# Optimization experiments

Measured on AMD Instinct MI355X. Metric: run time of the kernel, lower is better.

Reference implementation:

```python
import jax, jax.numpy as jnp
import numpy as np

BINS = 1024
DIM = 128
B, T = 8, 32768


def setup_inputs() -> dict:
    key = jax.random.key(0)
    k1, k2 = jax.random.split(key)
    hidden_states = jax.random.normal(k1, (B, T, DIM), dtype=jnp.float32)
    embed = jax.random.normal(k2, (BINS, DIM), dtype=jnp.float32)
    return {"hidden_states": hidden_states, "embed": embed}


def reference(hidden_states, embed):
    # encode: flatten to [N, dim], nearest codebook entry by Euclidean distance
    shape = hidden_states.shape
    x = hidden_states.reshape(-1, shape[-1])                    # [N, dim]
    x_sq = jnp.sum(x * x, axis=1, keepdims=True)                # [N, 1]
    e_sq = jnp.sum(embed * embed, axis=1)[None, :]              # [1, bins]
    dist = -(x_sq - 2.0 * (x @ embed.T) + e_sq)                 # [N, bins]
    embed_ind = jnp.argmax(dist, axis=-1)                       # [N]
    embed_ind = embed_ind.reshape(shape[:-1])                   # [B, T]
    # decode: embedding gather
    quantize = embed[embed_ind]                                 # [B, T, dim]
    return quantize, embed_ind
```

## Files before the change

kernel.cpp:

```cpp
#include <hip/hip_runtime.h>

#define DIM  128
#define BINS 1024

typedef __attribute__((ext_vector_type(8))) _Float16 f16x8;
typedef __attribute__((ext_vector_type(4))) float f32x4;

#define MFMA16(a, b, c) __builtin_amdgcn_mfma_f32_16x16x32_f16(a, b, c, 0, 0, 0)

#define GLDS(gp, lp) __builtin_amdgcn_global_load_lds(                        \
    (const __attribute__((address_space(1))) void*)(gp),                     \
    (__attribute__((address_space(3))) void*)(lp), 16, 0, 0)

__device__ __forceinline__ float med3a(float a, float b, float c) {
    float r;
    asm("v_med3_f32 %0, %1, %2, %3" : "=v"(r) : "v"(a), "v"(b), "v"(c));
    return r;
}

__device__ __forceinline__ float packkey(float k, int bin) {
    float r;
    asm("v_and_or_b32 %0, %1, %2, %3"
        : "=v"(r) : "v"(k), "s"(0xFFFFFC00u), "v"(bin));
    return r;
}

#define SINS(x, S0, S1, S2, S3) do {                                          \
        float n0_ = fmaxf(S0, (x));                                           \
        float n1_ = med3a((x), S0, S1);                                       \
        float n2_ = med3a((x), S1, S2);                                       \
        float n3_ = med3a((x), S2, S3);                                       \
        S0 = n0_; S1 = n1_; S2 = n2_; S3 = n3_;                               \
    } while (0)

__global__ __launch_bounds__(256) void vq_prep(
    const float* __restrict__ embed, _Float16* __restrict__ ehs,
    float* __restrict__ esq_g, float* __restrict__ cinit_g)
{
    int b = blockIdx.x * 256 + threadIdx.x;
    const float* e = embed + (size_t)b * DIM;
    float s = 0.f;
    #pragma unroll
    for (int k = 0; k < DIM; ++k) s = fmaf(e[k], e[k], s);
    esq_g[b] = s;
    cinit_g[b] = -0.5f * s;
    #pragma unroll
    for (int c = 0; c < 16; ++c) {
        int slot = c ^ (b & 15);
        #pragma unroll
        for (int j = 0; j < 8; ++j)
            ehs[b * 128 + slot * 8 + j] = (_Float16)e[c * 8 + j];
    }
}

__global__ __launch_bounds__(256) void vq_stage_a(
    const float* __restrict__ x,
    const _Float16* __restrict__ ehs_g,
    const float* __restrict__ cinit_g,
    float* __restrict__ cand)
{
    __shared__ _Float16 ehb[2][8192];
    __shared__ float ci_lds[BINS];

    const int tid = threadIdx.x;
    const int li  = tid & 15;
    const int g   = (tid >> 4) & 3;
    const int w   = tid >> 6;

    f16x8 xh[2][4];
    const size_t rowA = (size_t)blockIdx.x * 128 + w * 32 + li;
    #pragma unroll
    for (int rs = 0; rs < 2; ++rs) {
        const float* xp = x + (rowA + rs * 16) * DIM + g * 8;
        #pragma unroll
        for (int s = 0; s < 4; ++s) {
            float4 v0 = *(const float4*)(xp + s * 32);
            float4 v1 = *(const float4*)(xp + s * 32 + 4);
            f16x8 h;
            h[0] = (_Float16)v0.x; h[1] = (_Float16)v0.y;
            h[2] = (_Float16)v0.z; h[3] = (_Float16)v0.w;
            h[4] = (_Float16)v1.x; h[5] = (_Float16)v1.y;
            h[6] = (_Float16)v1.z; h[7] = (_Float16)v1.w;
            xh[rs][s] = h;
        }
    }

#define STAGE(stp_, buf_) do {                                                \
        const char* gE_ = (const char*)ehs_g + (size_t)(stp_) * 16384;        \
        char* lE_ = (char*)&ehb[buf_][0];                                     \
        _Pragma("unroll")                                                     \
        for (int j_ = 0; j_ < 4; ++j_) {                                      \
            int o_ = tid * 16 + j_ * 4096;                                    \
            GLDS(gE_ + o_, lE_ + o_);                                         \
        }                                                                     \
    } while (0)

    GLDS((const char*)cinit_g + tid * 16, (char*)ci_lds + tid * 16);
    STAGE(0, 0);
    asm volatile("s_waitcnt vmcnt(0)" ::: "memory");
    __syncthreads();

    const float NEG = __uint_as_float(0xFF7FFC00u);
    float s0[2], s1[2], s2[2], s3[2];
    #pragma unroll
    for (int rs = 0; rs < 2; ++rs) { s0[rs] = s1[rs] = s2[rs] = s3[rs] = NEG; }

#define LDE(tl_, s_) (*(const f16x8*)((const char*)&ehb[buf][0] + (tl_) * 4096 + li * 256 + (((g + 4 * (s_)) ^ li) << 4)))

    for (int stp = 0; stp < 16; ++stp) {
        const int buf = stp & 1;
        if (stp < 15) STAGE(stp + 1, buf ^ 1);

        #pragma unroll
        for (int tl = 0; tl < 4; ++tl) {
            const int binb = stp * 64 + tl * 16 + g * 4;
            const f32x4 ci = *(const f32x4*)&ci_lds[binb];
            f16x8 eh0 = LDE(tl, 0), eh1 = LDE(tl, 1);
            f16x8 eh2 = LDE(tl, 2), eh3 = LDE(tl, 3);
            f32x4 aP0 = MFMA16(eh0, xh[0][0], ci);
            f32x4 aP1 = MFMA16(eh0, xh[1][0], ci);
            aP0 = MFMA16(eh1, xh[0][1], aP0); aP1 = MFMA16(eh1, xh[1][1], aP1);
            aP0 = MFMA16(eh2, xh[0][2], aP0); aP1 = MFMA16(eh2, xh[1][2], aP1);
            aP0 = MFMA16(eh3, xh[0][3], aP0); aP1 = MFMA16(eh3, xh[1][3], aP1);
            {
                float p0 = packkey(aP0[0], binb + 0);
                float p1 = packkey(aP0[1], binb + 1);
                float p2 = packkey(aP0[2], binb + 2);
                float p3 = packkey(aP0[3], binb + 3);
                float pm01 = fmaxf(p0, p1), pm23 = fmaxf(p2, p3);
                SINS(pm01, s0[0], s1[0], s2[0], s3[0]);
                SINS(pm23, s0[0], s1[0], s2[0], s3[0]);
            }
            {
                float p0 = packkey(aP1[0], binb + 0);
                float p1 = packkey(aP1[1], binb + 1);
                float p2 = packkey(aP1[2], binb + 2);
                float p3 = packkey(aP1[3], binb + 3);
                float pm01 = fmaxf(p0, p1), pm23 = fmaxf(p2, p3);
                SINS(pm01, s0[1], s1[1], s2[1], s3[1]);
                SINS(pm23, s0[1], s1[1], s2[1], s3[1]);
            }
        }
        asm volatile("s_waitcnt vmcnt(0)" ::: "memory");
        __syncthreads();
    }
#undef LDE
#undef STAGE

    #pragma unroll
    for (int mm = 16; mm <= 32; mm <<= 1) {
        #pragma unroll
        for (int rs = 0; rs < 2; ++rs) {
            float q0 = __shfl_xor(s0[rs], mm);
            float q1 = __shfl_xor(s1[rs], mm);
            float q2 = __shfl_xor(s2[rs], mm);
            float q3 = __shfl_xor(s3[rs], mm);
            SINS(q0, s0[rs], s1[rs], s2[rs], s3[rs]);
            SINS(q1, s0[rs], s1[rs], s2[rs], s3[rs]);
            SINS(q2, s0[rs], s1[rs], s2[rs], s3[rs]);
            SINS(q3, s0[rs], s1[rs], s2[rs], s3[rs]);
        }
    }
    if ((tid & 63) < 16) {
        #pragma unroll
        for (int rs = 0; rs < 2; ++rs) {
            const size_t r = rowA + rs * 16;
            cand[r * 4 + 0] = (float)(__float_as_uint(s0[rs]) & 1022u);
            cand[r * 4 + 1] = (float)(__float_as_uint(s1[rs]) & 1022u);
            cand[r * 4 + 2] = (float)(__float_as_uint(s2[rs]) & 1022u);
            cand[r * 4 + 3] = (float)(__float_as_uint(s3[rs]) & 1022u);
        }
    }
}

__global__ __launch_bounds__(256) void vq_rescore(
    const float* __restrict__ x, const float* __restrict__ embed,
    const float* __restrict__ esq_g, const float* __restrict__ cand,
    float* __restrict__ ind_f, float4* __restrict__ outq)
{
    const int tid = threadIdx.x;
    const int sub = tid & 3;
    const size_t row = (size_t)blockIdx.x * 64 + (tid >> 2);

    const float4* xg = (const float4*)(x + row * DIM);
    float4 xq[8];
    #pragma unroll
    for (int j = 0; j < 8; ++j) xq[j] = xg[j * 4 + sub];

    float xs = 0.f;
    #pragma unroll
    for (int j = 0; j < 8; ++j) {
        float4 v = xq[j];
        xs = fmaf(v.x, v.x, xs); xs = fmaf(v.y, v.y, xs);
        xs = fmaf(v.z, v.z, xs); xs = fmaf(v.w, v.w, xs);
    }
    xs += __shfl_xor(xs, 1);
    xs += __shfl_xor(xs, 2);

    const float4 qv = *(const float4*)&cand[row * 4];
    const int qb0 = (int)qv.x, qb1 = (int)qv.y, qb2 = (int)qv.z, qb3 = (int)qv.w;

    const float4* e4 = (const float4*)embed;
    f32x4 acc[8];
    #pragma unroll
    for (int c = 0; c < 8; ++c) acc[c] = f32x4{0.f,0.f,0.f,0.f};
    #pragma unroll
    for (int c = 0; c < 8; ++c) {
        const int bin = (c < 2 ? qb0 : c < 4 ? qb1 : c < 6 ? qb2 : qb3) + (c & 1);
        #pragma unroll
        for (int j = 0; j < 8; ++j) {
            float4 ev = e4[(size_t)bin * 32 + j * 4 + sub];
            float4 xv = xq[j];
            acc[c][0] = fmaf(xv.x, ev.x, acc[c][0]);
            acc[c][1] = fmaf(xv.y, ev.y, acc[c][1]);
            acc[c][2] = fmaf(xv.z, ev.z, acc[c][2]);
            acc[c][3] = fmaf(xv.w, ev.w, acc[c][3]);
        }
    }
    float bd = -3.402823466e38f;
    int   bb = 0x7FFFFFFF;
    #pragma unroll
    for (int c = 0; c < 8; ++c) {
        const int bin = (c < 2 ? qb0 : c < 4 ? qb1 : c < 6 ? qb2 : qb3) + (c & 1);
        float p = (acc[c][0] + acc[c][1]) + (acc[c][2] + acc[c][3]);
        p += __shfl_xor(p, 1);
        p += __shfl_xor(p, 2);
        float d = -(fmaf(-2.f, p, xs) + esq_g[bin]);
        if (d > bd || (d == bd && bin < bb)) { bd = d; bb = bin; }
    }
    if (sub == 0) ind_f[row] = (float)bb;
    if (outq) {
        #pragma unroll
        for (int j = 0; j < 8; ++j)
            outq[row * 32 + j * 4 + sub] = e4[(size_t)bb * 32 + j * 4 + sub];
    }
}

__global__ __launch_bounds__(256) void vq_gather(
    const float* __restrict__ embed,
    const float* __restrict__ ind_f,
    float4* __restrict__ out)
{
    int i   = blockIdx.x * 256 + threadIdx.x;
    int row = i >> 5;
    int k   = i & 31;
    int b   = (int)ind_f[row];
    out[i] = reinterpret_cast<const float4*>(embed)[b * (DIM / 4) + k];
}

extern "C" void kernel_launch(void* const* d_in, const int* in_sizes, int n_in,
                              void* d_out, int out_size, void* d_ws, size_t ws_size,
                              hipStream_t stream) {
    const float* x     = (const float*)d_in[0];
    const float* embed = (const float*)d_in[1];
    float* out = (float*)d_out;

    const int N = in_sizes[0] / DIM;
    float* ind_f = out + (size_t)N * DIM;

    const bool use_ws = ws_size >= ((size_t)6 << 20);
    _Float16* ehs; float* esq_g; float* cinit_g; float* cand;
    if (use_ws) {
        char* wb = (char*)d_ws;
        ehs     = (_Float16*)wb;
        esq_g   = (float*)(wb + (256u << 10));
        cinit_g = (float*)(wb + (260u << 10));
        cand    = (float*)(wb + (512u << 10));
    } else {
        char* ob = (char*)d_out;
        cand    = out;
        ehs     = (_Float16*)(ob + (32u << 20));
        esq_g   = (float*)(ob + (36u << 20));
        cinit_g = (float*)(ob + (36u << 20) + 4096);
    }

    vq_prep<<<BINS / 256, 256, 0, stream>>>(embed, ehs, esq_g, cinit_g);
    vq_stage_a<<<N / 128, 256, 0, stream>>>(x, ehs, cinit_g, cand);
    vq_rescore<<<N / 64, 256, 0, stream>>>(x, embed, esq_g, cand, ind_f,
                                           use_ws ? (float4*)out : nullptr);
    if (!use_ws)
        vq_gather<<<(N * (DIM / 4)) / 256, 256, 0, stream>>>(embed, ind_f, (float4*)out);
}
```

Measured before the change: 188.5 us.

## Use 1024-thread blocks staging half the codebook at once in stage A

Stage A now runs 1024-thread blocks covering 512 rows, and loads half the fp16 codebook (128KB) into LDS in two phases instead of double-buffering 16KB slices with a barrier per slice. This cuts the number of barriers and reuses each staged codebook tile across four times as many rows. The cinit bias is read straight from global instead of LDS. The key packing now does the max of each bin pair before packing a 9-bit pair id, which saves packkey ops. The cost is a single block per CU with no overlap between loads and compute, and the coarser key gives less mantissa precision for the candidate shortlist.

```diff
diff --git a/kernel.cpp b/kernel.cpp
--- a/kernel.cpp
+++ b/kernel.cpp
@@ -18,10 +18,10 @@
     return r;
 }
 
-__device__ __forceinline__ float packkey(float k, int bin) {
+__device__ __forceinline__ float packkey(float k, int pid) {
     float r;
     asm("v_and_or_b32 %0, %1, %2, %3"
-        : "=v"(r) : "v"(k), "s"(0xFFFFFC00u), "v"(bin));
+        : "=v"(r) : "v"(k), "s"(0xFFFFFE00u), "v"(pid));
     return r;
 }
 
@@ -53,22 +53,22 @@
     }
 }
 
-__global__ __launch_bounds__(256) void vq_stage_a(
+__global__ __launch_bounds__(1024, 1) void vq_stage_a(
     const float* __restrict__ x,
     const _Float16* __restrict__ ehs_g,
     const float* __restrict__ cinit_g,
     float* __restrict__ cand)
 {
-    __shared__ _Float16 ehb[2][8192];
-    __shared__ float ci_lds[BINS];
-
-    const int tid = threadIdx.x;
-    const int li  = tid & 15;
-    const int g   = (tid >> 4) & 3;
-    const int w   = tid >> 6;
+    __shared__ _Float16 ehb[65536];
+
+    const int tid  = threadIdx.x;
+    const int lane = tid & 63;
+    const int li   = lane & 15;
+    const int g    = lane >> 4;
+    const int w    = tid >> 6;
 
     f16x8 xh[2][4];
-    const size_t rowA = (size_t)blockIdx.x * 128 + w * 32 + li;
+    const size_t rowA = (size_t)blockIdx.x * 512 + w * 32 + li;
     #pragma unroll
     for (int rs = 0; rs < 2; ++rs) {
         const float* xp = x + (rowA + rs * 16) * DIM + g * 8;
@@ -85,67 +85,59 @@
         }
     }
 
-#define STAGE(stp_, buf_) do {                                                \
-        const char* gE_ = (const char*)ehs_g + (size_t)(stp_) * 16384;        \
-        char* lE_ = (char*)&ehb[buf_][0];                                     \
-        _Pragma("unroll")                                                     \
-        for (int j_ = 0; j_ < 4; ++j_) {                                      \
-            int o_ = tid * 16 + j_ * 4096;                                    \
-            GLDS(gE_ + o_, lE_ + o_);                                         \
-        }                                                                     \
-    } while (0)
-
-    GLDS((const char*)cinit_g + tid * 16, (char*)ci_lds + tid * 16);
-    STAGE(0, 0);
-    asm volatile("s_waitcnt vmcnt(0)" ::: "memory");
-    __syncthreads();
-
-    const float NEG = __uint_as_float(0xFF7FFC00u);
+    int off0 = li * 256 + (((g + 0)  ^ li) << 4);
+    int off1 = li * 256 + (((g + 4)  ^ li) << 4);
+    int off2 = li * 256 + (((g + 8)  ^ li) << 4);
+    int off3 = li * 256 + (((g + 12) ^ li) << 4);
+    const float* cip = cinit_g + g * 4;
+
+    const float NEG = __uint_as_float(0xFF7FFE00u);
     float s0[2], s1[2], s2[2], s3[2];
     #pragma unroll
     for (int rs = 0; rs < 2; ++rs) { s0[rs] = s1[rs] = s2[rs] = s3[rs] = NEG; }
 
-#define LDE(tl_, s_) (*(const f16x8*)((const char*)&ehb[buf][0] + (tl_) * 4096 + li * 256 + (((g + 4 * (s_)) ^ li) << 4)))
-
-    for (int stp = 0; stp < 16; ++stp) {
-        const int buf = stp & 1;
-        if (stp < 15) STAGE(stp + 1, buf ^ 1);
-
-        #pragma unroll
-        for (int tl = 0; tl < 4; ++tl) {
-            const int binb = stp * 64 + tl * 16 + g * 4;
-            const f32x4 ci = *(const f32x4*)&ci_lds[binb];
-            f16x8 eh0 = LDE(tl, 0), eh1 = LDE(tl, 1);
-            f16x8 eh2 = LDE(tl, 2), eh3 = LDE(tl, 3);
-            f32x4 aP0 = MFMA16(eh0, xh[0][0], ci);
-            f32x4 aP1 = MFMA16(eh0, xh[1][0], ci);
-            aP0 = MFMA16(eh1, xh[0][1], aP0); aP1 = MFMA16(eh1, xh[1][1], aP1);
-            aP0 = MFMA16(eh2, xh[0][2], aP0); aP1 = MFMA16(eh2, xh[1][2], aP1);
-            aP0 = MFMA16(eh3, xh[0][3], aP0); aP1 = MFMA16(eh3, xh[1][3], aP1);
+    for (int p = 0; p < 2; ++p) {
+        if (p) __syncthreads();
+        {
+            const char* gsrc = (const char*)ehs_g + (size_t)p * 131072;
+            char* ldst = (char*)&ehb[0];
+            int o = tid * 16;
+            #pragma unroll
+            for (int sl = 0; sl < 8; ++sl)
+                GLDS(gsrc + sl * 16384 + o, ldst + sl * 16384 + o);
+        }
+        asm volatile("s_waitcnt vmcnt(0)" ::: "memory");
+        __syncthreads();
+
+        #pragma unroll 4
+        for (int tt = 0; tt < 32; ++tt) {
+            const int t = p * 32 + tt;
+            const char* bE = (const char*)&ehb[0] + tt * 4096;
+            f16x8 e0 = *(const f16x8*)(bE + off0);
+            f16x8 e1 = *(const f16x8*)(bE + off1);
+            f16x8 e2 = *(const f16x8*)(bE + off2);
+            f16x8 e3 = *(const f16x8*)(bE + off3);
+            const f32x4 ci = *(const f32x4*)(cip + t * 16);
+            f32x4 aP0 = MFMA16(e0, xh[0][0], ci);
+            f32x4 aP1 = MFMA16(e0, xh[1][0], ci);
+            aP0 = MFMA16(e1, xh[0][1], aP0); aP1 = MFMA16(e1, xh[1][1], aP1);
+            aP0 = MFMA16(e2, xh[0][2], aP0); aP1 = MFMA16(e2, xh[1][2], aP1);
+            aP0 = MFMA16(e3, xh[0][3], aP0); aP1 = MFMA16(e3, xh[1][3], aP1);
+            const int pid = t * 8 + g * 2;
             {
-                float p0 = packkey(aP0[0], binb + 0);
-                float p1 = packkey(aP0[1], binb + 1);
-                float p2 = packkey(aP0[2], binb + 2);
-                float p3 = packkey(aP0[3], binb + 3);
-                float pm01 = fmaxf(p0, p1), pm23 = fmaxf(p2, p3);
-                SINS(pm01, s0[0], s1[0], s2[0], s3[0]);
-                SINS(pm23, s0[0], s1[0], s2[0], s3[0]);
+                float q01 = packkey(fmaxf(aP0[0], aP0[1]), pid);
+                float q23 = packkey(fmaxf(aP0[2], aP0[3]), pid + 1);
+                SINS(q01, s0[0], s1[0], s2[0], s3[0]);
+                SINS(q23, s0[0], s1[0], s2[0], s3[0]);
             }
             {
-                float p0 = packkey(aP1[0], binb + 0);
-                float p1 = packkey(aP1[1], binb + 1);
-                float p2 = packkey(aP1[2], binb + 2);
-                float p3 = packkey(aP1[3], binb + 3);
-                float pm01 = fmaxf(p0, p1), pm23 = fmaxf(p2, p3);
-                SINS(pm01, s0[1], s1[1], s2[1], s3[1]);
-                SINS(pm23, s0[1], s1[1], s2[1], s3[1]);
+                float q01 = packkey(fmaxf(aP1[0], aP1[1]), pid);
+                float q23 = packkey(fmaxf(aP1[2], aP1[3]), pid + 1);
+                SINS(q01, s0[1], s1[1], s2[1], s3[1]);
+                SINS(q23, s0[1], s1[1], s2[1], s3[1]);
             }
         }
-        asm volatile("s_waitcnt vmcnt(0)" ::: "memory");
-        __syncthreads();
-    }
-#undef LDE
-#undef STAGE
+    }
 
     #pragma unroll
     for (int mm = 16; mm <= 32; mm <<= 1) {
@@ -161,14 +153,14 @@
             SINS(q3, s0[rs], s1[rs], s2[rs], s3[rs]);
         }
     }
-    if ((tid & 63) < 16) {
+    if (lane < 16) {
         #pragma unroll
         for (int rs = 0; rs < 2; ++rs) {
             const size_t r = rowA + rs * 16;
-            cand[r * 4 + 0] = (float)(__float_as_uint(s0[rs]) & 1022u);
-            cand[r * 4 + 1] = (float)(__float_as_uint(s1[rs]) & 1022u);
-            cand[r * 4 + 2] = (float)(__float_as_uint(s2[rs]) & 1022u);
-            cand[r * 4 + 3] = (float)(__float_as_uint(s3[rs]) & 1022u);
+            cand[r * 4 + 0] = (float)((__float_as_uint(s0[rs]) & 0x1FFu) << 1);
+            cand[r * 4 + 1] = (float)((__float_as_uint(s1[rs]) & 0x1FFu) << 1);
+            cand[r * 4 + 2] = (float)((__float_as_uint(s2[rs]) & 0x1FFu) << 1);
+            cand[r * 4 + 3] = (float)((__float_as_uint(s3[rs]) & 0x1FFu) << 1);
         }
     }
 }
@@ -275,7 +267,7 @@
     }
 
     vq_prep<<<BINS / 256, 256, 0, stream>>>(embed, ehs, esq_g, cinit_g);
-    vq_stage_a<<<N / 128, 256, 0, stream>>>(x, ehs, cinit_g, cand);
+    vq_stage_a<<<N / 512, 1024, 0, stream>>>(x, ehs, cinit_g, cand);
     vq_rescore<<<N / 64, 256, 0, stream>>>(x, embed, esq_g, cand, ind_f,
                                            use_ws ? (float4*)out : nullptr);
     if (!use_ws)
```

After: 190.0 us. No clear change (+0.8%).
